# Optimization experiments

Hardware: AMD Instinct MI355X
Metric: run time of the kernel (lower is better)

## Reference

```python
import jax, jax.numpy as jnp
import numpy as np

B, H, Wd, C = 8, 64, 64, 128
KH, KW = 3, 3
N = KH * KW  # kernel_n
F = 256


def _grid_offset(h, w, kh, kw):
    """Replicates the TensorLayer grid construction exactly, including the
    (2,kh,kw)->(kh*kw,2) reshape of the stacked meshgrid."""
    n = kh * kw
    initial = np.stack(np.meshgrid(np.arange(kh), np.arange(kw), indexing='ij'))  # (2,kh,kw)
    initial = initial.reshape(-1, 2).astype(np.float32)  # (n,2), faithful flattening order
    gy = np.arange(-int((kh - 1) / 2.0), h - int((kh - 1) / 2.0))
    gx = np.arange(-int((kw - 1) / 2.0), w - int((kw - 1) / 2.0))
    grid = np.stack(np.meshgrid(gy, gx, indexing='ij'), axis=-1).astype(np.float32)  # (h,w,2)
    grid = np.tile(grid[:, :, None, :], (1, 1, n, 1))  # (h,w,n,2)
    return jnp.asarray(grid + initial[None, None, :, :])  # (h,w,n,2)


def setup_inputs() -> dict:
    key = jax.random.key(0)
    k1, k2, k3 = jax.random.split(key, 3)
    x = jax.random.normal(k1, (B, H, Wd, C), dtype=jnp.float32)
    offsets = jax.random.normal(k2, (B, H, Wd, 2 * N), dtype=jnp.float32)
    W = jax.random.normal(k3, (N, C, F), dtype=jnp.float32) * 0.02  # truncated_normal(0.02) analogue
    b = jnp.zeros((F,), dtype=jnp.float32)
    return {"x": x, "offsets": offsets, "W": W, "b": b}


def reference(x, offsets, W, b):
    h, w = x.shape[1], x.shape[2]
    grid = _grid_offset(h, w, KH, KW)  # (h,w,n,2)
    coords = grid[None] + offsets.reshape(x.shape[0], h, w, N, 2)  # (b,h,w,n,2)
    cy = jnp.clip(coords[..., 0], 0.0, jnp.float32(h - 1))
    cx = jnp.clip(coords[..., 1], 0.0, jnp.float32(w - 1))
    y0 = jnp.floor(cy).astype(jnp.int32)
    y1 = jnp.ceil(cy).astype(jnp.int32)
    x0 = jnp.floor(cx).astype(jnp.int32)
    x1 = jnp.ceil(cx).astype(jnp.int32)

    bidx = jnp.arange(x.shape[0])[:, None, None, None]

    def gather(yy, xx):
        return x[bidx, yy, xx]  # (b,h,w,n,c)

    v_lt = gather(y0, x0)
    v_rb = gather(y1, x1)
    v_lb = gather(y0, x1)  # (lt_y, rb_x) as in original
    v_rt = gather(y1, x0)  # (rb_y, lt_x) as in original

    fy = (cy - y0.astype(cy.dtype))[..., None]
    fx = (cx - x0.astype(cx.dtype))[..., None]
    vals_t = v_lt + (v_rt - v_lt) * fy
    vals_b = v_lb + (v_rb - v_lb) * fy
    mapped = vals_t + (vals_b - vals_t) * fx  # (b,h,w,n,c)

    # conv3d with kernel [1,1,n,c,f] + VALID == contraction over (n,c)
    out = jnp.einsum('bhwnc,ncf->bhwf', mapped, W) + b
    return out
```

## Files before the change

### kernel.cpp

```cpp
#include <hip/hip_runtime.h>

#define HH 64
#define WW 64
#define CC 128
#define FF 256
#define NTAP 9
#define KD 1152
#define XELEMS (8 * HH * WW * CC)
#define XCVT_BLOCKS (XELEMS / (256 * 8))
#define WT_BLOCKS 144

typedef __attribute__((ext_vector_type(8))) short bf16x8;
typedef __attribute__((ext_vector_type(4))) float floatx4;

__device__ inline unsigned short f2bf(float v) {
  union { float f; unsigned u; } c; c.f = v;
  unsigned r = (c.u + 0x7FFFu + ((c.u >> 16) & 1u)) >> 16;
  return (unsigned short)r;
}
__device__ inline float bflo(unsigned u) {
  union { unsigned u; float f; } c; c.u = u << 16; return c.f;
}
__device__ inline float bfhi(unsigned u) {
  union { unsigned u; float f; } c; c.u = u & 0xFFFF0000u; return c.f;
}
__device__ inline unsigned cvt_pk_bf16(float lo, float hi) {
  unsigned r;
  asm("v_cvt_pk_bf16_f32 %0, %1, %2" : "=v"(r) : "v"(lo), "v"(hi));
  return r;
}

__device__ inline unsigned lerp_word(unsigned u00, unsigned u10, unsigned u01, unsigned u11,
                                     float w00, float w10, float w01, float w11) {
  float rlo = bflo(u00) * w00 + bflo(u10) * w10 + bflo(u01) * w01 + bflo(u11) * w11;
  float rhi = bfhi(u00) * w00 + bfhi(u10) * w10 + bfhi(u01) * w01 + bfhi(u11) * w11;
  return cvt_pk_bf16(rlo, rhi);
}

__device__ inline void block_sync_lds() {
  __builtin_amdgcn_sched_barrier(0);
  asm volatile("s_waitcnt lgkmcnt(0)\n\ts_barrier" ::: "memory");
  __builtin_amdgcn_sched_barrier(0);
}

#define IY_PACK 0x18690
#define IX_PACK 0x21894

struct ITap { int b00, b10, b01, b11; float fy, fx; };

__device__ inline ITap tap_from(float2 o2, int yy, int xx, int n) {
  float cy = (float)(yy - 1 + ((IY_PACK >> (2 * n)) & 3)) + o2.x;
  float cx = (float)(xx - 1 + ((IX_PACK >> (2 * n)) & 3)) + o2.y;
  cy = fminf(fmaxf(cy, 0.f), 63.f);
  cx = fminf(fmaxf(cx, 0.f), 63.f);
  const float fy0 = floorf(cy), fx0 = floorf(cx);
  const int y0 = (int)fy0, y1 = (int)ceilf(cy);
  const int x0 = (int)fx0, x1 = (int)ceilf(cx);
  ITap t;
  t.b00 = (y0 * WW + x0) * CC;
  t.b10 = (y1 * WW + x0) * CC;
  t.b01 = (y0 * WW + x1) * CC;
  t.b11 = (y1 * WW + x1) * CC;
  t.fy = cy - fy0;
  t.fx = cx - fx0;
  return t;
}

__global__ void prep_kernel(const float* __restrict__ X, const float* __restrict__ W,
                            unsigned short* __restrict__ Xb, unsigned short* __restrict__ Wtf) {
  const int blk = blockIdx.x;
  if (blk < XCVT_BLOCKS) {
    const int t = blk * 256 + threadIdx.x;
    const float4* src = (const float4*)(X + (size_t)t * 8);
    float4 a = src[0], b2 = src[1];
    bf16x8 o;
    o[0] = (short)f2bf(a.x);  o[1] = (short)f2bf(a.y);
    o[2] = (short)f2bf(a.z);  o[3] = (short)f2bf(a.w);
    o[4] = (short)f2bf(b2.x); o[5] = (short)f2bf(b2.y);
    o[6] = (short)f2bf(b2.z); o[7] = (short)f2bf(b2.w);
    *(bf16x8*)(Xb + (size_t)t * 8) = o;
  } else {
    const int t = (blk - XCVT_BLOCKS) * 256 + threadIdx.x;
    const int f  = t & 255;
    const int kc = t >> 8;
    unsigned short o[8];
#pragma unroll
    for (int j = 0; j < 8; ++j)
      o[j] = f2bf(W[(size_t)(kc * 8 + j) * FF + f]);
    const int kt = kc >> 3, ks = (kc >> 2) & 1, aq = kc & 3;
    const int fg = f >> 6, ft = (f >> 4) & 3, arow = f & 15;
    const size_t addr = (size_t)((kt * 2 + ks) * 16 + fg * 4 + ft) * 512 + aq * 128 + arow * 8;
    *(uint4*)(Wtf + addr) = *(uint4*)o;
  }
}

__global__ __launch_bounds__(512, 2) void fused_kernel(
    const unsigned short* __restrict__ Xb, const float* __restrict__ Off,
    const unsigned short* __restrict__ Wtf, const float* __restrict__ bias,
    float* __restrict__ Out)
{
  __shared__ unsigned short smA[2][64 * 64];

  const int blk = blockIdx.x;
  const int b   = blk & 7;
  const int y   = blk >> 3;
  const int m0  = b * 4096 + y * 64;
  const int tid = threadIdx.x;
  const int wave = tid >> 6, lane = tid & 63;

  if (wave < 4) {
    const int arow = lane & 15, aq = lane >> 4;
    const unsigned short* wbase = Wtf + (size_t)wave * 2048 + (size_t)lane * 8;

    floatx4 acc[4][4];
#pragma unroll
    for (int mt = 0; mt < 4; ++mt)
#pragma unroll
      for (int ft = 0; ft < 4; ++ft)
        acc[mt][ft] = (floatx4){0.f, 0.f, 0.f, 0.f};

    block_sync_lds();

    int cur = 0;
    for (int kt = 0; kt < 18; ++kt) {
      const unsigned short* wk = wbase + (size_t)kt * 16384;

      bf16x8 b0[4], b1[4];
#pragma unroll
      for (int ft = 0; ft < 4; ++ft)
        b0[ft] = *(const bf16x8*)(wk + ft * 512);

      bf16x8 afr[2][4];
#pragma unroll
      for (int ks = 0; ks < 2; ++ks) {
        const int slot = (((ks * 4 + aq) ^ (arow & 7)) << 3);
#pragma unroll
        for (int mt = 0; mt < 4; ++mt)
          afr[ks][mt] = *(const bf16x8*)&smA[cur][(mt * 16 + arow) * 64 + slot];
      }

#pragma unroll
      for (int ft = 0; ft < 4; ++ft)
        b1[ft] = *(const bf16x8*)(wk + 8192 + ft * 512);

      __builtin_amdgcn_s_setprio(1);
#pragma unroll
      for (int mt = 0; mt < 4; ++mt)
#pragma unroll
        for (int ft = 0; ft < 4; ++ft)
          acc[mt][ft] = __builtin_amdgcn_mfma_f32_16x16x32_bf16(
              afr[0][mt], b0[ft], acc[mt][ft], 0, 0, 0);
#pragma unroll
      for (int mt = 0; mt < 4; ++mt)
#pragma unroll
        for (int ft = 0; ft < 4; ++ft)
          acc[mt][ft] = __builtin_amdgcn_mfma_f32_16x16x32_bf16(
              afr[1][mt], b1[ft], acc[mt][ft], 0, 0, 0);
      __builtin_amdgcn_s_setprio(0);

      block_sync_lds();
      cur ^= 1;
    }

    float bv[4];
#pragma unroll
    for (int ft = 0; ft < 4; ++ft)
      bv[ft] = bias[wave * 64 + ft * 16 + arow];
#pragma unroll
    for (int mt = 0; mt < 4; ++mt) {
#pragma unroll
      for (int ft = 0; ft < 4; ++ft) {
        const int f = wave * 64 + ft * 16 + arow;
#pragma unroll
        for (int r = 0; r < 4; ++r) {
          const int m = m0 + mt * 16 + aq * 4 + r;
          Out[(size_t)m * FF + f] = acc[mt][ft][r] + bv[ft];
        }
      }
    }
  } else {
    const int ptid = tid & 255;
    const int p    = ptid >> 2;
    const int c0   = ptid & 3;

    const unsigned short* xb = Xb + (size_t)b * (HH * WW * CC);
    const float* offp = Off + ((size_t)(b * HH + y) * WW + p) * (2 * NTAP);

    const int sa0 = p * 64 + ((c0 ^ (p & 7)) << 3);
    const int sa1 = p * 64 + (((c0 + 4) ^ (p & 7)) << 3);

    ITap tL = tap_from(*(const float2*)offp, y, p, 0);
    uint4 g[2][4];
    {
      const float gy = 1.f - tL.fy, gx = 1.f - tL.fx;
      const float w00 = gy * gx, w10 = tL.fy * gx, w01 = gy * tL.fx, w11 = tL.fy * tL.fx;
#pragma unroll
      for (int cc = 0; cc < 2; ++cc) {
        const int ch = (c0 + cc * 4) * 8;
        uint4 q00 = *(const uint4*)(xb + tL.b00 + ch);
        uint4 q10 = *(const uint4*)(xb + tL.b10 + ch);
        uint4 q01 = *(const uint4*)(xb + tL.b01 + ch);
        uint4 q11 = *(const uint4*)(xb + tL.b11 + ch);
        uint4 o;
        o.x = lerp_word(q00.x, q10.x, q01.x, q11.x, w00, w10, w01, w11);
        o.y = lerp_word(q00.y, q10.y, q01.y, q11.y, w00, w10, w01, w11);
        o.z = lerp_word(q00.z, q10.z, q01.z, q11.z, w00, w10, w01, w11);
        o.w = lerp_word(q00.w, q10.w, q01.w, q11.w, w00, w10, w01, w11);
        *(uint4*)&smA[0][cc ? sa1 : sa0] = o;
      }
#pragma unroll
      for (int cc = 0; cc < 2; ++cc) {
        const int ch1 = (8 + c0 + cc * 4) * 8;
        g[cc][0] = *(const uint4*)(xb + tL.b00 + ch1);
        g[cc][1] = *(const uint4*)(xb + tL.b10 + ch1);
        g[cc][2] = *(const uint4*)(xb + tL.b01 + ch1);
        g[cc][3] = *(const uint4*)(xb + tL.b11 + ch1);
      }
    }
    ITap tG = tL;
    block_sync_lds();

    int cur = 0;
    for (int kt = 0; kt < 18; ++kt) {
      uint4 gn[2][4];
      if (kt <= 15) {
        if ((kt & 1) == 0)
          tG = tap_from(*(const float2*)(offp + 2 * ((kt + 2) >> 1)), y, p, (kt + 2) >> 1);
#pragma unroll
        for (int cc = 0; cc < 2; ++cc) {
          const int ch = ((kt & 1) * 8 + c0 + cc * 4) * 8;
          gn[cc][0] = *(const uint4*)(xb + tG.b00 + ch);
          gn[cc][1] = *(const uint4*)(xb + tG.b10 + ch);
          gn[cc][2] = *(const uint4*)(xb + tG.b01 + ch);
          gn[cc][3] = *(const uint4*)(xb + tG.b11 + ch);
        }
      }

      if (kt <= 16) {
        const float gy = 1.f - tL.fy, gx = 1.f - tL.fx;
        const float w00 = gy * gx, w10 = tL.fy * gx, w01 = gy * tL.fx, w11 = tL.fy * tL.fx;
#pragma unroll
        for (int cc = 0; cc < 2; ++cc) {
          uint4 o;
          o.x = lerp_word(g[cc][0].x, g[cc][1].x, g[cc][2].x, g[cc][3].x, w00, w10, w01, w11);
          o.y = lerp_word(g[cc][0].y, g[cc][1].y, g[cc][2].y, g[cc][3].y, w00, w10, w01, w11);
          o.z = lerp_word(g[cc][0].z, g[cc][1].z, g[cc][2].z, g[cc][3].z, w00, w10, w01, w11);
          o.w = lerp_word(g[cc][0].w, g[cc][1].w, g[cc][2].w, g[cc][3].w, w00, w10, w01, w11);
          *(uint4*)&smA[cur ^ 1][cc ? sa1 : sa0] = o;
        }
      }

      if (kt <= 15) {
#pragma unroll
        for (int cc = 0; cc < 2; ++cc)
#pragma unroll
          for (int q2 = 0; q2 < 4; ++q2)
            g[cc][q2] = gn[cc][q2];
      }

      block_sync_lds();
      cur ^= 1;
      tL = tG;
    }
  }
}

extern "C" void kernel_launch(void* const* d_in, const int* in_sizes, int n_in,
                              void* d_out, int out_size, void* d_ws, size_t ws_size,
                              hipStream_t stream) {
  const float* X    = (const float*)d_in[0];
  const float* Off  = (const float*)d_in[1];
  const float* W    = (const float*)d_in[2];
  const float* bias = (const float*)d_in[3];
  float* Out = (float*)d_out;

  unsigned short* Wtf = (unsigned short*)d_ws;
  unsigned short* Xb  = Wtf + (size_t)FF * KD;

  prep_kernel<<<XCVT_BLOCKS + WT_BLOCKS, 256, 0, stream>>>(X, W, Xb, Wtf);
  fused_kernel<<<512, 512, 0, stream>>>(Xb, Off, Wtf, bias, Out);
}
```

Measured before the change: 113.1 us.

## Replace block barriers with LDS flag counters and a 4-deep stage ring

Replaces the per-iteration workgroup barriers between producer (gather/lerp) waves and consumer (MFMA) waves with per-stage LDS counters. Producers increment a produced count, consumers poll and then increment a release count, and the LDS A buffer grows from 2 to 4 stages so producers can run up to three tiles ahead. The consumer also hoists both weight fragment loads ahead of the wait. This aims to decouple the two wave groups and remove lock-step stalls, at the cost of spin-polling LDS with s_sleep, more shared memory, and reliance on memory ordering around the flags.

Result: slower. 115.7 us (+2.3%).

```diff
diff --git a/kernel.cpp b/kernel.cpp
--- a/kernel.cpp
+++ b/kernel.cpp
@@ -37,10 +37,13 @@
   return cvt_pk_bf16(rlo, rhi);
 }
 
-__device__ inline void block_sync_lds() {
-  __builtin_amdgcn_sched_barrier(0);
-  asm volatile("s_waitcnt lgkmcnt(0)\n\ts_barrier" ::: "memory");
-  __builtin_amdgcn_sched_barrier(0);
+__device__ inline void poll_ge(const int* p, int v) {
+  while (*(volatile const int*)p < v) __builtin_amdgcn_s_sleep(2);
+  asm volatile("" ::: "memory");
+}
+__device__ inline void flag_inc(int* p, int lane) {
+  asm volatile("s_waitcnt lgkmcnt(0)" ::: "memory");
+  if (lane == 0) atomicAdd(p, 1);
 }
 
 #define IY_PACK 0x18690
@@ -99,7 +102,9 @@
     const unsigned short* __restrict__ Wtf, const float* __restrict__ bias,
     float* __restrict__ Out)
 {
-  __shared__ unsigned short smA[2][64 * 64];
+  __shared__ unsigned short smA[4][64 * 64];
+  __shared__ int prodcnt[18];
+  __shared__ int relcnt[18];
 
   const int blk = blockIdx.x;
   const int b   = blk & 7;
@@ -108,6 +113,9 @@
   const int tid = threadIdx.x;
   const int wave = tid >> 6, lane = tid & 63;
 
+  if (tid < 18) { prodcnt[tid] = 0; relcnt[tid] = 0; }
+  __syncthreads();
+
   if (wave < 4) {
     const int arow = lane & 15, aq = lane >> 4;
     const unsigned short* wbase = Wtf + (size_t)wave * 2048 + (size_t)lane * 8;
@@ -119,29 +127,29 @@
       for (int ft = 0; ft < 4; ++ft)
         acc[mt][ft] = (floatx4){0.f, 0.f, 0.f, 0.f};
 
-    block_sync_lds();
-
-    int cur = 0;
-    for (int kt = 0; kt < 18; ++kt) {
-      const unsigned short* wk = wbase + (size_t)kt * 16384;
+    for (int t = 0; t < 18; ++t) {
+      const unsigned short* wk = wbase + (size_t)t * 16384;
 
       bf16x8 b0[4], b1[4];
 #pragma unroll
       for (int ft = 0; ft < 4; ++ft)
         b0[ft] = *(const bf16x8*)(wk + ft * 512);
+#pragma unroll
+      for (int ft = 0; ft < 4; ++ft)
+        b1[ft] = *(const bf16x8*)(wk + 8192 + ft * 512);
+
+      poll_ge(&prodcnt[t], 4);
 
       bf16x8 afr[2][4];
+      const unsigned short* sa = smA[t & 3];
 #pragma unroll
       for (int ks = 0; ks < 2; ++ks) {
         const int slot = (((ks * 4 + aq) ^ (arow & 7)) << 3);
 #pragma unroll
         for (int mt = 0; mt < 4; ++mt)
-          afr[ks][mt] = *(const bf16x8*)&smA[cur][(mt * 16 + arow) * 64 + slot];
-      }
-
-#pragma unroll
-      for (int ft = 0; ft < 4; ++ft)
-        b1[ft] = *(const bf16x8*)(wk + 8192 + ft * 512);
+          afr[ks][mt] = *(const bf16x8*)&sa[(mt * 16 + arow) * 64 + slot];
+      }
+      flag_inc(&relcnt[t], lane);
 
       __builtin_amdgcn_s_setprio(1);
 #pragma unroll
@@ -157,9 +165,6 @@
           acc[mt][ft] = __builtin_amdgcn_mfma_f32_16x16x32_bf16(
               afr[1][mt], b1[ft], acc[mt][ft], 0, 0, 0);
       __builtin_amdgcn_s_setprio(0);
-
-      block_sync_lds();
-      cur ^= 1;
     }
 
     float bv[4];
@@ -208,6 +213,7 @@
         o.w = lerp_word(q00.w, q10.w, q01.w, q11.w, w00, w10, w01, w11);
         *(uint4*)&smA[0][cc ? sa1 : sa0] = o;
       }
+      flag_inc(&prodcnt[0], lane);
 #pragma unroll
       for (int cc = 0; cc < 2; ++cc) {
         const int ch1 = (8 + c0 + cc * 4) * 8;
@@ -218,10 +224,10 @@
       }
     }
     ITap tG = tL;
-    block_sync_lds();
-
-    int cur = 0;
-    for (int kt = 0; kt < 18; ++kt) {
+
+    for (int kt = 0; kt < 17; ++kt) {
+      const int pt = kt + 1;
+
       uint4 gn[2][4];
       if (kt <= 15) {
         if ((kt & 1) == 0)
@@ -236,9 +242,12 @@
         }
       }
 
-      if (kt <= 16) {
+      if (pt >= 4) poll_ge(&relcnt[pt - 4], 4);
+
+      {
         const float gy = 1.f - tL.fy, gx = 1.f - tL.fx;
         const float w00 = gy * gx, w10 = tL.fy * gx, w01 = gy * tL.fx, w11 = tL.fy * tL.fx;
+        unsigned short* sa = smA[pt & 3];
 #pragma unroll
         for (int cc = 0; cc < 2; ++cc) {
           uint4 o;
@@ -246,9 +255,10 @@
           o.y = lerp_word(g[cc][0].y, g[cc][1].y, g[cc][2].y, g[cc][3].y, w00, w10, w01, w11);
           o.z = lerp_word(g[cc][0].z, g[cc][1].z, g[cc][2].z, g[cc][3].z, w00, w10, w01, w11);
           o.w = lerp_word(g[cc][0].w, g[cc][1].w, g[cc][2].w, g[cc][3].w, w00, w10, w01, w11);
-          *(uint4*)&smA[cur ^ 1][cc ? sa1 : sa0] = o;
+          *(uint4*)&sa[cc ? sa1 : sa0] = o;
         }
       }
+      flag_inc(&prodcnt[pt], lane);
 
       if (kt <= 15) {
 #pragma unroll
@@ -257,9 +267,6 @@
           for (int q2 = 0; q2 < 4; ++q2)
             g[cc][q2] = gn[cc][q2];
       }
-
-      block_sync_lds();
-      cur ^= 1;
       tL = tG;
     }
   }
```
